# Optimization experiments

Hardware: AMD Instinct MI355X
Metric: run time of the kernel (lower is better)

The kernel has to match this reference:

```python
import jax, jax.numpy as jnp
import numpy as np

OUT = 7          # out_size
SCALE = 0.125    # spatial_scale (1/8, FPN P3)
SAMPLES = 2      # sample_num


def setup_inputs() -> dict:
    key = jax.random.key(0)
    k1, k2, k3, k4, k5, k6, k7, k8, k9 = jax.random.split(key, 9)
    B, C, H, W = 2, 256, 256, 256
    n = 1024
    features = jax.random.normal(k1, (B, C, H, W), jnp.float32)
    # rois: (batch_idx, cx, cy, w, h, theta) in IMAGE coordinates
    bidx = jax.random.randint(k2, (n,), 0, B).astype(jnp.float32)
    cx = jax.random.uniform(k3, (n,), jnp.float32, 0.0, W / SCALE)
    cy = jax.random.uniform(k4, (n,), jnp.float32, 0.0, H / SCALE)
    rw = jax.random.uniform(k5, (n,), jnp.float32, 16.0, 512.0)
    rh = jax.random.uniform(k6, (n,), jnp.float32, 16.0, 512.0)
    ang = jax.random.uniform(k7, (n,), jnp.float32, -np.pi, np.pi)
    rois = jnp.stack([bidx, cx, cy, rw, rh, ang], axis=1)
    ic = OUT * OUT * C  # 12544
    fc = 1024
    w1 = jax.random.normal(k8, (ic, fc), jnp.float32) * 0.01
    b1 = jnp.zeros((fc,), jnp.float32)
    w2 = jax.random.normal(k9, (fc, OUT * OUT), jnp.float32) * 0.01
    b2 = jnp.zeros((OUT * OUT,), jnp.float32)
    return {"features": features, "rois": rois, "w1": w1, "b1": b1, "w2": w2, "b2": b2}


def _roi_align_rotated(features, rois):
    B, C, H, W = features.shape
    n = rois.shape[0]
    bidx = rois[:, 0].astype(jnp.int32)
    cx = rois[:, 1] * SCALE
    cy = rois[:, 2] * SCALE
    rw = jnp.maximum(rois[:, 3] * SCALE, 1.0)
    rh = jnp.maximum(rois[:, 4] * SCALE, 1.0)
    theta = rois[:, 5]
    bin_w = rw / OUT
    bin_h = rh / OUT
    g = jnp.arange(OUT, dtype=features.dtype)
    s = (jnp.arange(SAMPLES, dtype=features.dtype) + 0.5) / SAMPLES
    # roi-local sample coordinates: [n, OUT, SAMPLES]
    yy = -rh[:, None, None] / 2 + (g[None, :, None] + s[None, None, :]) * bin_h[:, None, None]
    xx = -rw[:, None, None] / 2 + (g[None, :, None] + s[None, None, :]) * bin_w[:, None, None]
    # broadcast to [n, oh, ow, sy, sx]
    yy = yy[:, :, None, :, None]
    xx = xx[:, None, :, None, :]
    ct = jnp.cos(theta)[:, None, None, None, None]
    st = jnp.sin(theta)[:, None, None, None, None]
    xs = xx * ct - yy * st + cx[:, None, None, None, None]
    ys = xx * st + yy * ct + cy[:, None, None, None, None]
    shp = (n, OUT, OUT, SAMPLES, SAMPLES)
    xs = jnp.broadcast_to(xs, shp).reshape(n, -1)  # [n, P], P = OUT*OUT*S*S
    ys = jnp.broadcast_to(ys, shp).reshape(n, -1)
    valid = (ys > -1.0) & (ys < H) & (xs > -1.0) & (xs < W)
    ysc = jnp.clip(ys, 0.0, H - 1)
    xsc = jnp.clip(xs, 0.0, W - 1)
    yl = jnp.floor(ysc).astype(jnp.int32)
    xl = jnp.floor(xsc).astype(jnp.int32)
    yh = jnp.minimum(yl + 1, H - 1)
    xh = jnp.minimum(xl + 1, W - 1)
    ly = ysc - yl
    lx = xsc - xl
    hy = 1.0 - ly
    hx = 1.0 - lx
    be = jnp.broadcast_to(bidx[:, None], yl.shape)
    # bilinear gathers: each [n, P, C]
    v11 = features[be, :, yl, xl]
    v12 = features[be, :, yl, xh]
    v21 = features[be, :, yh, xl]
    v22 = features[be, :, yh, xh]
    val = ((hy * hx)[..., None] * v11 + (hy * lx)[..., None] * v12
           + (ly * hx)[..., None] * v21 + (ly * lx)[..., None] * v22)
    val = val * valid[..., None].astype(val.dtype)
    # average the SAMPLES*SAMPLES points per bin -> [n, OUT, OUT, C]
    val = val.reshape(n, OUT, OUT, SAMPLES * SAMPLES, C).mean(axis=3)
    return jnp.transpose(val, (0, 3, 1, 2))  # [n, C, OUT, OUT]


def reference(features, rois, w1, b1, w2, b2):
    n = rois.shape[0]
    x = _roi_align_rotated(features, rois)          # [n, C, OUT, OUT]
    flat = x.reshape(n, -1)                          # [n, C*OUT*OUT]
    hid = jax.nn.relu(flat @ w1 + b1)
    mask = jax.nn.sigmoid(hid @ w2 + b2).reshape(n, 1, OUT, OUT)
    return x * mask
```

## Files before the change

### kernel.cpp

```cpp
#include <hip/hip_runtime.h>
#include <hip/hip_bf16.h>

typedef unsigned short u16;
typedef short short8 __attribute__((ext_vector_type(8)));
typedef float f32x4 __attribute__((ext_vector_type(4)));

#define OUTD 7
#define NROI 1024
#define CH 256
#define HH 256
#define WW 256
#define KDIM 12544
#define NHID 1024
#define KSPLIT 8

__global__ __launch_bounds__(256) void transpose_feat(const float* __restrict__ f,
                                                      __hip_bfloat16* __restrict__ ft) {
    __shared__ float tile[32][33];
    int pb = blockIdx.x;
    int cb = blockIdx.y;
    int b  = blockIdx.z;
    int tx = threadIdx.x & 31;
    int ty = threadIdx.x >> 5;
    const float* src = f + ((size_t)(b * CH + cb * 32)) * 65536 + (size_t)pb * 32;
#pragma unroll
    for (int i = 0; i < 4; ++i) {
        int c = ty + i * 8;
        tile[c][tx] = src[(size_t)c * 65536 + tx];
    }
    __syncthreads();
    __hip_bfloat16* dst = ft + ((size_t)b * 65536 + (size_t)pb * 32) * CH + cb * 32;
#pragma unroll
    for (int i = 0; i < 4; ++i) {
        int p = ty + i * 8;
        dst[(size_t)p * CH + tx] = __float2bfloat16(tile[tx][p]);
    }
}

__global__ __launch_bounds__(256) void transpose_w1(const float* __restrict__ w1,
                                                    __hip_bfloat16* __restrict__ w1t) {
    __shared__ float tile[32][33];
    int kb = blockIdx.x;
    int nb = blockIdx.y;
    int tx = threadIdx.x & 31;
    int ty = threadIdx.x >> 5;
#pragma unroll
    for (int i = 0; i < 4; ++i) {
        int k = ty + i * 8;
        tile[k][tx] = w1[(size_t)(kb * 32 + k) * NHID + nb * 32 + tx];
    }
    __syncthreads();
#pragma unroll
    for (int i = 0; i < 4; ++i) {
        int nn = ty + i * 8;
        w1t[(size_t)(nb * 32 + nn) * KDIM + kb * 32 + tx] = __float2bfloat16(tile[tx][nn]);
    }
}

__global__ __launch_bounds__(256) void roi_align(const __hip_bfloat16* __restrict__ ft,
                                                 const float* __restrict__ rois,
                                                 float* __restrict__ x,
                                                 __hip_bfloat16* __restrict__ flat) {
    __shared__ float sbuf[KDIM];
    int i = blockIdx.x;
    int c = threadIdx.x;
    float r0 = rois[i * 6 + 0], r1 = rois[i * 6 + 1], r2 = rois[i * 6 + 2];
    float r3 = rois[i * 6 + 3], r4 = rois[i * 6 + 4], th = rois[i * 6 + 5];
    int b = (int)r0;
    float cx = r1 * 0.125f, cy = r2 * 0.125f;
    float rw = fmaxf(r3 * 0.125f, 1.0f), rh = fmaxf(r4 * 0.125f, 1.0f);
    float bw = rw * (1.0f / 7.0f), bh = rh * (1.0f / 7.0f);
    float ct = cosf(th), st = sinf(th);
    const __hip_bfloat16* fb = ft + (size_t)b * 65536 * CH;

    for (int bin = 0; bin < 49; ++bin) {
        int ph = bin / 7, pw = bin - (bin / 7) * 7;
        float acc = 0.f;
#pragma unroll
        for (int s = 0; s < 4; ++s) {
            int sy = s >> 1, sx2 = s & 1;
            float yy = -rh * 0.5f + ((float)ph + ((float)sy + 0.5f) * 0.5f) * bh;
            float xx = -rw * 0.5f + ((float)pw + ((float)sx2 + 0.5f) * 0.5f) * bw;
            float xs = xx * ct - yy * st + cx;
            float ys = xx * st + yy * ct + cy;
            bool valid = (ys > -1.0f) && (ys < 256.0f) && (xs > -1.0f) && (xs < 256.0f);
            float ysc = fminf(fmaxf(ys, 0.f), 255.f);
            float xsc = fminf(fmaxf(xs, 0.f), 255.f);
            int yl = (int)floorf(ysc), xl = (int)floorf(xsc);
            int yh = min(yl + 1, 255), xh = min(xl + 1, 255);
            float ly = ysc - (float)yl, lx = xsc - (float)xl;
            float hy = 1.f - ly, hx = 1.f - lx;
            const __hip_bfloat16* p11 = fb + ((size_t)(yl * 256 + xl) << 8);
            const __hip_bfloat16* p12 = fb + ((size_t)(yl * 256 + xh) << 8);
            const __hip_bfloat16* p21 = fb + ((size_t)(yh * 256 + xl) << 8);
            const __hip_bfloat16* p22 = fb + ((size_t)(yh * 256 + xh) << 8);
            float v = hy * hx * __bfloat162float(p11[c]) + hy * lx * __bfloat162float(p12[c])
                    + ly * hx * __bfloat162float(p21[c]) + ly * lx * __bfloat162float(p22[c]);
            acc += valid ? v : 0.f;
        }
        sbuf[c * 49 + bin] = acc * 0.25f;
    }
    __syncthreads();
    size_t base = (size_t)i * KDIM;
    for (int j = threadIdx.x; j < KDIM; j += 256) {
        float v = sbuf[j];
        x[base + j] = v;
        flat[base + j] = __float2bfloat16(v);
    }
}

__global__ __launch_bounds__(256) void gemm1(const u16* __restrict__ A,
                                             const u16* __restrict__ Bt,
                                             float* __restrict__ part) {
    const int K = KDIM;
    int nb = blockIdx.x, mb = blockIdx.y, ks = blockIdx.z;
    int steps = 24 + (ks < 4 ? 1 : 0);
    int kbase = (ks * 24 + (ks < 4 ? ks : 4)) * 64;
    __shared__ u16 As[128 * 64];
    __shared__ u16 Bs[128 * 64];
    int tid = threadIdx.x;
    int lane = tid & 63, w = tid >> 6;
    int wm = w >> 1, wn = w & 1;
    f32x4 acc[4][4] = {};
    const u16* Ab = A + (size_t)(mb * 128) * K;
    const u16* Bb = Bt + (size_t)(nb * 128) * K;

    for (int s = 0; s < steps; ++s) {
        int kk = kbase + s * 64;
        __syncthreads();
#pragma unroll
        for (int j = 0; j < 4; ++j) {
            int cid = tid + 256 * j;
            int row = cid >> 3, pq = cid & 7;
            int q = pq ^ (row & 7);
            uint4 va = *(const uint4*)(Ab + (size_t)row * K + kk + q * 8);
            *(uint4*)(As + row * 64 + pq * 8) = va;
            uint4 vb = *(const uint4*)(Bb + (size_t)row * K + kk + q * 8);
            *(uint4*)(Bs + row * 64 + pq * 8) = vb;
        }
        __syncthreads();
#pragma unroll
        for (int kh = 0; kh < 2; ++kh) {
            short8 af[4], bf[4];
#pragma unroll
            for (int t = 0; t < 4; ++t) {
                int q = kh * 4 + (lane >> 4);
                int r = wm * 64 + t * 16 + (lane & 15);
                int pq = q ^ (r & 7);
                af[t] = *(const short8*)(As + r * 64 + pq * 8);
                int rb = wn * 64 + t * 16 + (lane & 15);
                int pqb = q ^ (rb & 7);
                bf[t] = *(const short8*)(Bs + rb * 64 + pqb * 8);
            }
#pragma unroll
            for (int mt = 0; mt < 4; ++mt)
#pragma unroll
                for (int nt = 0; nt < 4; ++nt)
                    acc[mt][nt] = __builtin_amdgcn_mfma_f32_16x16x32_bf16(af[mt], bf[nt], acc[mt][nt], 0, 0, 0);
        }
    }
    float* P = part + (size_t)ks * NROI * NHID;
    int m_base = mb * 128 + wm * 64, n_base = nb * 128 + wn * 64;
#pragma unroll
    for (int mt = 0; mt < 4; ++mt)
#pragma unroll
        for (int nt = 0; nt < 4; ++nt)
#pragma unroll
            for (int i = 0; i < 4; ++i) {
                int m = m_base + mt * 16 + (lane >> 4) * 4 + i;
                int n = n_base + nt * 16 + (lane & 15);
                P[(size_t)m * NHID + n] = acc[mt][nt][i];
            }
}

__global__ __launch_bounds__(256) void reduce_relu(const float* __restrict__ part,
                                                   const float* __restrict__ b1,
                                                   float* __restrict__ hid) {
    int idx = blockIdx.x * 256 + threadIdx.x;
    float s = b1[idx & (NHID - 1)];
#pragma unroll
    for (int j = 0; j < KSPLIT; ++j) s += part[(size_t)j * NROI * NHID + idx];
    hid[idx] = fmaxf(s, 0.f);
}

__global__ __launch_bounds__(64) void gemm2_mask(const float* __restrict__ hid,
                                                 const float* __restrict__ w2,
                                                 const float* __restrict__ b2,
                                                 float* __restrict__ mask) {
    __shared__ float hrow[NHID];
    int i = blockIdx.x;
    for (int k = threadIdx.x; k < NHID; k += 64) hrow[k] = hid[(size_t)i * NHID + k];
    __syncthreads();
    int j = threadIdx.x;
    if (j < 49) {
        float acc = b2[j];
        for (int k = 0; k < NHID; ++k) acc += hrow[k] * w2[(size_t)k * 49 + j];
        mask[i * 49 + j] = 1.f / (1.f + expf(-acc));
    }
}

__global__ __launch_bounds__(256) void apply_mask(float* __restrict__ out,
                                                  const float* __restrict__ mask) {
    int idx = blockIdx.x * 256 + threadIdx.x;
    int i = idx / KDIM;
    int r = idx - i * KDIM;
    int p = r % 49;
    out[idx] = out[idx] * mask[i * 49 + p];
}

extern "C" void kernel_launch(void* const* d_in, const int* in_sizes, int n_in,
                              void* d_out, int out_size, void* d_ws, size_t ws_size,
                              hipStream_t stream) {
    const float* features = (const float*)d_in[0];
    const float* rois     = (const float*)d_in[1];
    const float* w1       = (const float*)d_in[2];
    const float* b1       = (const float*)d_in[3];
    const float* w2       = (const float*)d_in[4];
    const float* b2       = (const float*)d_in[5];
    float* out = (float*)d_out;
    char* ws = (char*)d_ws;

    __hip_bfloat16* featT = (__hip_bfloat16*)(ws);
    __hip_bfloat16* flat  = (__hip_bfloat16*)(ws + 67108864);
    __hip_bfloat16* w1t   = (__hip_bfloat16*)(ws + 92798976);
    float* part           = (float*)(ws + 118489088);
    float* hid            = (float*)(ws + 152043520);
    float* mask           = (float*)(ws + 156237824);

    transpose_feat<<<dim3(2048, 8, 2), 256, 0, stream>>>(features, featT);
    transpose_w1<<<dim3(392, 32), 256, 0, stream>>>(w1, w1t);
    roi_align<<<NROI, 256, 0, stream>>>(featT, rois, out, flat);
    gemm1<<<dim3(8, 8, KSPLIT), 256, 0, stream>>>((const u16*)flat, (const u16*)w1t, part);
    reduce_relu<<<4096, 256, 0, stream>>>(part, b1, hid);
    gemm2_mask<<<NROI, 64, 0, stream>>>(hid, w2, b2, mask);
    apply_mask<<<50176, 256, 0, stream>>>(out, mask);
}
```

Measured before the change: 447.1 us.

## Vectorize transposes, roi_align gathers, reduction and mask application

Widens the feature and w1 transpose kernels to float4 loads and packed 4xbf16 stores over larger tiles. roi_align now has each wavefront own a subset of bins and each lane gather 4 channels with 8-byte loads, writing through a padded shared buffer. reduce_relu and apply_mask switch to float4 accesses, and apply_mask caches the 49 mask values per ROI in shared memory. The aim is fewer, wider memory transactions in the bandwidth-bound stages; the risk is that roi_align runs only 4 bins in parallel per block, which may expose more gather latency.

```diff
diff --git a/kernel.cpp b/kernel.cpp
--- a/kernel.cpp
+++ b/kernel.cpp
@@ -8,62 +8,84 @@
 #define OUTD 7
 #define NROI 1024
 #define CH 256
-#define HH 256
-#define WW 256
 #define KDIM 12544
 #define NHID 1024
 #define KSPLIT 8
 
+__device__ __forceinline__ float bf2f(u16 u) {
+    union { unsigned int i; float f; } v; v.i = ((unsigned int)u) << 16; return v.f;
+}
+__device__ __forceinline__ u16 f2b(float f) {
+    return (u16)(__bfloat16_as_ushort(__float2bfloat16(f)));
+}
+
 __global__ __launch_bounds__(256) void transpose_feat(const float* __restrict__ f,
-                                                      __hip_bfloat16* __restrict__ ft) {
-    __shared__ float tile[32][33];
+                                                      u16* __restrict__ ft) {
+    __shared__ float tile[32][129];
     int pb = blockIdx.x;
     int cb = blockIdx.y;
     int b  = blockIdx.z;
-    int tx = threadIdx.x & 31;
-    int ty = threadIdx.x >> 5;
-    const float* src = f + ((size_t)(b * CH + cb * 32)) * 65536 + (size_t)pb * 32;
-#pragma unroll
-    for (int i = 0; i < 4; ++i) {
-        int c = ty + i * 8;
-        tile[c][tx] = src[(size_t)c * 65536 + tx];
-    }
-    __syncthreads();
-    __hip_bfloat16* dst = ft + ((size_t)b * 65536 + (size_t)pb * 32) * CH + cb * 32;
-#pragma unroll
-    for (int i = 0; i < 4; ++i) {
-        int p = ty + i * 8;
-        dst[(size_t)p * CH + tx] = __float2bfloat16(tile[tx][p]);
+    int tid = threadIdx.x;
+    const float* src = f + ((size_t)(b * CH + cb * 32)) * 65536 + (size_t)pb * 128;
+#pragma unroll
+    for (int i = 0; i < 4; ++i) {
+        int id = tid + 256 * i;
+        int c = id >> 5, f4 = id & 31;
+        float4 v = *(const float4*)(src + (size_t)c * 65536 + f4 * 4);
+        tile[c][f4 * 4 + 0] = v.x;
+        tile[c][f4 * 4 + 1] = v.y;
+        tile[c][f4 * 4 + 2] = v.z;
+        tile[c][f4 * 4 + 3] = v.w;
+    }
+    __syncthreads();
+    u16* dst = ft + ((size_t)(b * 65536 + pb * 128)) * CH + cb * 32;
+#pragma unroll
+    for (int i = 0; i < 4; ++i) {
+        int id = tid + 256 * i;
+        int px = id >> 3, cg = id & 7;
+        uint2 o;
+        o.x = (unsigned)f2b(tile[cg * 4 + 0][px]) | ((unsigned)f2b(tile[cg * 4 + 1][px]) << 16);
+        o.y = (unsigned)f2b(tile[cg * 4 + 2][px]) | ((unsigned)f2b(tile[cg * 4 + 3][px]) << 16);
+        *(uint2*)(dst + (size_t)px * CH + cg * 4) = o;
     }
 }
 
 __global__ __launch_bounds__(256) void transpose_w1(const float* __restrict__ w1,
-                                                    __hip_bfloat16* __restrict__ w1t) {
-    __shared__ float tile[32][33];
+                                                    u16* __restrict__ w1t) {
+    __shared__ float tile[32][129];
     int kb = blockIdx.x;
     int nb = blockIdx.y;
-    int tx = threadIdx.x & 31;
-    int ty = threadIdx.x >> 5;
-#pragma unroll
-    for (int i = 0; i < 4; ++i) {
-        int k = ty + i * 8;
-        tile[k][tx] = w1[(size_t)(kb * 32 + k) * NHID + nb * 32 + tx];
-    }
-    __syncthreads();
-#pragma unroll
-    for (int i = 0; i < 4; ++i) {
-        int nn = ty + i * 8;
-        w1t[(size_t)(nb * 32 + nn) * KDIM + kb * 32 + tx] = __float2bfloat16(tile[tx][nn]);
-    }
-}
-
-__global__ __launch_bounds__(256) void roi_align(const __hip_bfloat16* __restrict__ ft,
+    int tid = threadIdx.x;
+#pragma unroll
+    for (int i = 0; i < 4; ++i) {
+        int id = tid + 256 * i;
+        int r = id >> 3, f4 = id & 7;
+        float4 v = *(const float4*)(w1 + (size_t)(kb * 128 + r) * NHID + nb * 32 + f4 * 4);
+        tile[f4 * 4 + 0][r] = v.x;
+        tile[f4 * 4 + 1][r] = v.y;
+        tile[f4 * 4 + 2][r] = v.z;
+        tile[f4 * 4 + 3][r] = v.w;
+    }
+    __syncthreads();
+#pragma unroll
+    for (int i = 0; i < 4; ++i) {
+        int id = tid + 256 * i;
+        int nn = id >> 5, kg = id & 31;
+        uint2 o;
+        o.x = (unsigned)f2b(tile[nn][kg * 4 + 0]) | ((unsigned)f2b(tile[nn][kg * 4 + 1]) << 16);
+        o.y = (unsigned)f2b(tile[nn][kg * 4 + 2]) | ((unsigned)f2b(tile[nn][kg * 4 + 3]) << 16);
+        *(uint2*)(w1t + (size_t)(nb * 32 + nn) * KDIM + kb * 128 + kg * 4) = o;
+    }
+}
+
+__global__ __launch_bounds__(256) void roi_align(const u16* __restrict__ ft,
                                                  const float* __restrict__ rois,
                                                  float* __restrict__ x,
-                                                 __hip_bfloat16* __restrict__ flat) {
-    __shared__ float sbuf[KDIM];
+                                                 u16* __restrict__ flat) {
+    __shared__ float sbuf[49 * 257];
     int i = blockIdx.x;
-    int c = threadIdx.x;
+    int tid = threadIdx.x;
+    int lane = tid & 63, w = tid >> 6;
     float r0 = rois[i * 6 + 0], r1 = rois[i * 6 + 1], r2 = rois[i * 6 + 2];
     float r3 = rois[i * 6 + 3], r4 = rois[i * 6 + 4], th = rois[i * 6 + 5];
     int b = (int)r0;
@@ -71,11 +93,15 @@
     float rw = fmaxf(r3 * 0.125f, 1.0f), rh = fmaxf(r4 * 0.125f, 1.0f);
     float bw = rw * (1.0f / 7.0f), bh = rh * (1.0f / 7.0f);
     float ct = cosf(th), st = sinf(th);
-    const __hip_bfloat16* fb = ft + (size_t)b * 65536 * CH;
-
-    for (int bin = 0; bin < 49; ++bin) {
-        int ph = bin / 7, pw = bin - (bin / 7) * 7;
-        float acc = 0.f;
+    const u16* fb = ft + (size_t)b * 65536 * CH;
+    int coff = lane * 4;
+
+    int start = w * 12 + (w > 0 ? 1 : 0);
+    int cnt = (w == 0) ? 13 : 12;
+    for (int bi = 0; bi < cnt; ++bi) {
+        int bin = start + bi;
+        int ph = bin / 7, pw = bin - ph * 7;
+        float a0 = 0.f, a1 = 0.f, a2 = 0.f, a3 = 0.f;
 #pragma unroll
         for (int s = 0; s < 4; ++s) {
             int sy = s >> 1, sx2 = s & 1;
@@ -90,22 +116,33 @@
             int yh = min(yl + 1, 255), xh = min(xl + 1, 255);
             float ly = ysc - (float)yl, lx = xsc - (float)xl;
             float hy = 1.f - ly, hx = 1.f - lx;
-            const __hip_bfloat16* p11 = fb + ((size_t)(yl * 256 + xl) << 8);
-            const __hip_bfloat16* p12 = fb + ((size_t)(yl * 256 + xh) << 8);
-            const __hip_bfloat16* p21 = fb + ((size_t)(yh * 256 + xl) << 8);
-            const __hip_bfloat16* p22 = fb + ((size_t)(yh * 256 + xh) << 8);
-            float v = hy * hx * __bfloat162float(p11[c]) + hy * lx * __bfloat162float(p12[c])
-                    + ly * hx * __bfloat162float(p21[c]) + ly * lx * __bfloat162float(p22[c]);
-            acc += valid ? v : 0.f;
+            float w11 = hy * hx, w12 = hy * lx, w21 = ly * hx, w22 = ly * lx;
+            if (!valid) { w11 = w12 = w21 = w22 = 0.f; }
+            uint2 v11 = *(const uint2*)(fb + (((size_t)yl * 256 + xl) << 8) + coff);
+            uint2 v12 = *(const uint2*)(fb + (((size_t)yl * 256 + xh) << 8) + coff);
+            uint2 v21 = *(const uint2*)(fb + (((size_t)yh * 256 + xl) << 8) + coff);
+            uint2 v22 = *(const uint2*)(fb + (((size_t)yh * 256 + xh) << 8) + coff);
+            a0 += w11 * bf2f(v11.x & 0xffff) + w12 * bf2f(v12.x & 0xffff)
+                + w21 * bf2f(v21.x & 0xffff) + w22 * bf2f(v22.x & 0xffff);
+            a1 += w11 * bf2f(v11.x >> 16)    + w12 * bf2f(v12.x >> 16)
+                + w21 * bf2f(v21.x >> 16)    + w22 * bf2f(v22.x >> 16);
+            a2 += w11 * bf2f(v11.y & 0xffff) + w12 * bf2f(v12.y & 0xffff)
+                + w21 * bf2f(v21.y & 0xffff) + w22 * bf2f(v22.y & 0xffff);
+            a3 += w11 * bf2f(v11.y >> 16)    + w12 * bf2f(v12.y >> 16)
+                + w21 * bf2f(v21.y >> 16)    + w22 * bf2f(v22.y >> 16);
         }
-        sbuf[c * 49 + bin] = acc * 0.25f;
+        float* sb = sbuf + bin * 257 + coff;
+        sb[0] = a0 * 0.25f; sb[1] = a1 * 0.25f; sb[2] = a2 * 0.25f; sb[3] = a3 * 0.25f;
     }
     __syncthreads();
     size_t base = (size_t)i * KDIM;
-    for (int j = threadIdx.x; j < KDIM; j += 256) {
-        float v = sbuf[j];
-        x[base + j] = v;
-        flat[base + j] = __float2bfloat16(v);
+#pragma unroll 1
+    for (int k = 0; k < 49; ++k) {
+        int o = tid + k * 256;
+        int c = o / 49, bin = o - c * 49;
+        float v = sbuf[bin * 257 + c];
+        x[base + o] = v;
+        flat[base + o] = f2b(v);
     }
 }
 
@@ -176,11 +213,19 @@
 __global__ __launch_bounds__(256) void reduce_relu(const float* __restrict__ part,
                                                    const float* __restrict__ b1,
                                                    float* __restrict__ hid) {
-    int idx = blockIdx.x * 256 + threadIdx.x;
-    float s = b1[idx & (NHID - 1)];
-#pragma unroll
-    for (int j = 0; j < KSPLIT; ++j) s += part[(size_t)j * NROI * NHID + idx];
-    hid[idx] = fmaxf(s, 0.f);
+    int idx4 = blockIdx.x * 256 + threadIdx.x;
+    const float4* pv = (const float4*)part;
+    const float4* bv = (const float4*)b1;
+    float4 s = bv[idx4 & 255];
+#pragma unroll
+    for (int j = 0; j < KSPLIT; ++j) {
+        float4 p = pv[(size_t)j * 262144 + idx4];
+        s.x += p.x; s.y += p.y; s.z += p.z; s.w += p.w;
+    }
+    float4 r;
+    r.x = fmaxf(s.x, 0.f); r.y = fmaxf(s.y, 0.f);
+    r.z = fmaxf(s.z, 0.f); r.w = fmaxf(s.w, 0.f);
+    ((float4*)hid)[idx4] = r;
 }
 
 __global__ __launch_bounds__(64) void gemm2_mask(const float* __restrict__ hid,
@@ -201,11 +246,23 @@
 
 __global__ __launch_bounds__(256) void apply_mask(float* __restrict__ out,
                                                   const float* __restrict__ mask) {
-    int idx = blockIdx.x * 256 + threadIdx.x;
-    int i = idx / KDIM;
-    int r = idx - i * KDIM;
-    int p = r % 49;
-    out[idx] = out[idx] * mask[i * 49 + p];
+    __shared__ float mrow[49];
+    int i = blockIdx.x;
+    int tid = threadIdx.x;
+    if (tid < 49) mrow[tid] = mask[i * 49 + tid];
+    __syncthreads();
+    float4* o = (float4*)(out + (size_t)i * KDIM);
+#pragma unroll 1
+    for (int idx = tid; idx < 3136; idx += 256) {
+        float4 v = o[idx];
+        int e = idx * 4;
+        int p = e % 49;
+        v.x *= mrow[p]; if (++p == 49) p = 0;
+        v.y *= mrow[p]; if (++p == 49) p = 0;
+        v.z *= mrow[p]; if (++p == 49) p = 0;
+        v.w *= mrow[p];
+        o[idx] = v;
+    }
 }
 
 extern "C" void kernel_launch(void* const* d_in, const int* in_sizes, int n_in,
@@ -220,18 +277,18 @@
     float* out = (float*)d_out;
     char* ws = (char*)d_ws;
 
-    __hip_bfloat16* featT = (__hip_bfloat16*)(ws);
-    __hip_bfloat16* flat  = (__hip_bfloat16*)(ws + 67108864);
-    __hip_bfloat16* w1t   = (__hip_bfloat16*)(ws + 92798976);
-    float* part           = (float*)(ws + 118489088);
-    float* hid            = (float*)(ws + 152043520);
-    float* mask           = (float*)(ws + 156237824);
-
-    transpose_feat<<<dim3(2048, 8, 2), 256, 0, stream>>>(features, featT);
-    transpose_w1<<<dim3(392, 32), 256, 0, stream>>>(w1, w1t);
+    u16* featT  = (u16*)(ws);
+    u16* flat   = (u16*)(ws + 67108864);
+    u16* w1t    = (u16*)(ws + 92798976);
+    float* part = (float*)(ws + 118489088);
+    float* hid  = (float*)(ws + 152043520);
+    float* mask = (float*)(ws + 156237824);
+
+    transpose_feat<<<dim3(512, 8, 2), 256, 0, stream>>>(features, featT);
+    transpose_w1<<<dim3(98, 32), 256, 0, stream>>>(w1, w1t);
     roi_align<<<NROI, 256, 0, stream>>>(featT, rois, out, flat);
-    gemm1<<<dim3(8, 8, KSPLIT), 256, 0, stream>>>((const u16*)flat, (const u16*)w1t, part);
-    reduce_relu<<<4096, 256, 0, stream>>>(part, b1, hid);
+    gemm1<<<dim3(8, 8, KSPLIT), 256, 0, stream>>>(flat, w1t, part);
+    reduce_relu<<<1024, 256, 0, stream>>>(part, b1, hid);
     gemm2_mask<<<NROI, 64, 0, stream>>>(hid, w2, b2, mask);
-    apply_mask<<<50176, 256, 0, stream>>>(out, mask);
-}
+    apply_mask<<<NROI, 256, 0, stream>>>(out, mask);
+}
```

Measured after the change: 417.8 us. 1.07x faster.
